# Kernel optimization log

Hardware: AMD Instinct MI355X
Metric: run time of the kernel (lower is better)

Reference implementation:

```python
import jax, jax.numpy as jnp
import numpy as np

N = 1_000_000
G = 32
CLAMP = 1e-4          # sigmoid_clamp
GAMMA = 2.0           # module-level gamma
FOCAL_ALPHA = 0.25    # cfg.MODEL.FCOS.LOSS_ALPHA
FOCAL_GAMMA = 2.0     # cfg.MODEL.FCOS.LOSS_GAMMA


def setup_inputs() -> dict:
    key = jax.random.key(0)
    k1, k2, k3, k4 = jax.random.split(key, 4)
    return {
        "logits_pred": jax.random.normal(k1, (N, 1), dtype=jnp.float32),
        "scores": jax.random.uniform(k2, (N, 1), dtype=jnp.float32),
        "IoUMap": jax.random.uniform(k3, (N, 1), dtype=jnp.float32),
        "is_in_boxes": jax.random.randint(k4, (N, G), 0, 2, dtype=jnp.int32),
        "num_pos_avg": 100,
    }


def reference(logits_pred, scores, IoUMap, is_in_boxes, num_pos_avg):
    f32 = jnp.float32
    mask = is_in_boxes > 0                                  # [N,G] bool
    any_mask = mask.any(axis=0)                             # [G]

    p = jnp.clip(jax.nn.sigmoid(logits_pred), CLAMP, 1.0 - CLAMP)  # box_pred [N,1]
    p0 = p[:, 0]                                            # [N]

    # alignment metrics: single class => scores[:, labels] broadcasts column 0
    am = scores[:, 0][:, None] * mask.astype(f32)           # [N,G]
    iou = jax.lax.stop_gradient(IoUMap)[:, 0][:, None] * mask.astype(f32)

    # per-box confidence = max of alignment metric over in-box locations
    conf = jnp.max(jnp.where(mask, am, -jnp.inf), axis=0)   # [G]
    conf = jnp.where(any_mask, conf, f32(0.0))

    am_safe = jnp.where(mask, am, f32(1.0))                 # avoid pow(0, c) grad issues
    raw = jnp.where(mask, jnp.power(am_safe, conf[None, :]) * iou, f32(0.0))

    # normalize(x) = (x + 1e-4) / (max(x) + 1e-4) over in-box subset
    mx = jnp.max(jnp.where(mask, raw, -jnp.inf), axis=0)    # [G]
    mx = jnp.where(any_mask, mx, f32(1.0))
    pos_w = jnp.where(mask & any_mask[None, :],
                      (raw + CLAMP) / (mx[None, :] + CLAMP), f32(0.0))  # [N,G]

    # negative mask: locations covered by no gt box (single-class case)
    neg_mask = ~mask.any(axis=1)                            # [N]
    neg_loss = jnp.sum(jnp.where(neg_mask,
                                 -jnp.log(1.0 - p0) * jnp.power(p0, FOCAL_GAMMA),
                                 f32(0.0))) * (1.0 - FOCAL_ALPHA)

    wmask = pos_w > 0.0
    wc = jnp.clip(pos_w, CLAMP, 1.0 - CLAMP)                # clamp applied at positive entries
    logp = jnp.log(p0)[:, None]
    log1mp = jnp.log(1.0 - p0)[:, None]
    pos_loss = -jnp.sum(jnp.where(wmask,
                                  logp * jnp.power(wc * (1.0 - p0)[:, None], GAMMA),
                                  f32(0.0))) * FOCAL_ALPHA
    box_neg_loss = -jnp.sum(jnp.where(wmask,
                                      log1mp * jnp.power((1.0 - wc) * p0[:, None], GAMMA),
                                      f32(0.0))) * FOCAL_ALPHA

    denom = jnp.asarray(num_pos_avg, f32)
    return (neg_loss + pos_loss + box_neg_loss) / denom
```

## Files before the change

kernel.cpp:

```cpp
#include <hip/hip_runtime.h>
#include <hip/hip_bf16.h>
#include <stdint.h>


constexpr float kClamp = 1e-4f;
constexpr uint32_t kNegInfKey = 0x007FFFFFu;

__device__ inline uint32_t fkey(float f) {
    uint32_t u = __float_as_uint(f);
    return (u & 0x80000000u) ? ~u : (u | 0x80000000u);
}
__device__ inline float funkey(uint32_t k) {
    uint32_t u = (k & 0x80000000u) ? (k ^ 0x80000000u) : ~k;
    return __uint_as_float(u);
}

__global__ void init_kernel(uint32_t* confbits, uint32_t* mxkeys, float* out) {
    int t = threadIdx.x;
    if (t < 32) { confbits[t] = 0u; mxkeys[t] = kNegInfKey; }
    if (t == 0) out[0] = 0.0f;
}

template <bool WRITE_BITS>
__global__ void pack_conf_kernel(const int4* __restrict__ boxes4,
                                 const float* __restrict__ scores,
                                 uint32_t* __restrict__ bits,
                                 uint32_t* __restrict__ confbits,
                                 long long nchunks) {
    __shared__ uint32_t conf_lds[32];
    int tid = threadIdx.x;
    if (tid < 32) conf_lds[tid] = 0u;
    __syncthreads();
    int g0 = (tid & 7) * 4;
    float r0 = 0.0f, r1 = 0.0f, r2 = 0.0f, r3 = 0.0f;
    long long stride = (long long)gridDim.x * blockDim.x;
    for (long long c = (long long)blockIdx.x * blockDim.x + tid; c < nchunks; c += stride) {
        int4 v = boxes4[c];
        uint32_t nib = (uint32_t)(v.x > 0) | ((uint32_t)(v.y > 0) << 1) |
                       ((uint32_t)(v.z > 0) << 2) | ((uint32_t)(v.w > 0) << 3);
        long long row = c >> 3;
        if (WRITE_BITS) {
            uint32_t r = nib << ((tid & 7) * 4);
            r |= __shfl_xor(r, 1);
            r |= __shfl_xor(r, 2);
            r |= __shfl_xor(r, 4);
            if ((tid & 7) == 0) bits[row] = r;
        }
        float s = scores[row];
        r0 = (nib & 1u) ? fmaxf(r0, s) : r0;
        r1 = (nib & 2u) ? fmaxf(r1, s) : r1;
        r2 = (nib & 4u) ? fmaxf(r2, s) : r2;
        r3 = (nib & 8u) ? fmaxf(r3, s) : r3;
    }
    for (int off = 8; off < 64; off <<= 1) {
        r0 = fmaxf(r0, __shfl_xor(r0, off));
        r1 = fmaxf(r1, __shfl_xor(r1, off));
        r2 = fmaxf(r2, __shfl_xor(r2, off));
        r3 = fmaxf(r3, __shfl_xor(r3, off));
    }
    if ((tid & 63) < 8) {
        atomicMax(&conf_lds[g0 + 0], __float_as_uint(r0));
        atomicMax(&conf_lds[g0 + 1], __float_as_uint(r1));
        atomicMax(&conf_lds[g0 + 2], __float_as_uint(r2));
        atomicMax(&conf_lds[g0 + 3], __float_as_uint(r3));
    }
    __syncthreads();
    if (tid < 32 && conf_lds[tid]) atomicMax(&confbits[tid], conf_lds[tid]);
}

__device__ inline uint32_t row_mask_from_boxes(const int4* __restrict__ boxes4, int row) {
    uint32_t m = 0;
#pragma unroll
    for (int k = 0; k < 8; ++k) {
        int4 v = boxes4[(long long)row * 8 + k];
        uint32_t nib = (uint32_t)(v.x > 0) | ((uint32_t)(v.y > 0) << 1) |
                       ((uint32_t)(v.z > 0) << 2) | ((uint32_t)(v.w > 0) << 3);
        m |= nib << (k * 4);
    }
    return m;
}

template <bool USE_BITS>
__global__ void mx_kernel(const uint32_t* __restrict__ bits,
                          const int4* __restrict__ boxes4,
                          const float* __restrict__ scores,
                          const float* __restrict__ iouMap,
                          const uint32_t* __restrict__ confbits,
                          uint32_t* __restrict__ mxkeys, int n) {
    __shared__ float conf_s[32];
    __shared__ float smax_w[4][32];
    int tid = threadIdx.x;
    if (tid < 32) conf_s[tid] = __uint_as_float(confbits[tid]);
    __syncthreads();
    int chunk = tid & 3;
    float cf[8];
#pragma unroll
    for (int k = 0; k < 8; ++k) cf[k] = conf_s[chunk * 8 + k];
    float lmax[8];
#pragma unroll
    for (int k = 0; k < 8; ++k) lmax[k] = -__builtin_inff();

    int slots = (gridDim.x * blockDim.x) >> 2;
    for (int row = (blockIdx.x * blockDim.x + tid) >> 2; row < n; row += slots) {
        uint32_t m = USE_BITS ? bits[row] : row_mask_from_boxes(boxes4, row);
        uint32_t mc = (m >> (chunk * 8)) & 0xFFu;
        if (!mc) continue;
        float l2s = log2f(scores[row]);
        float l2i = log2f(iouMap[row]);
#pragma unroll
        for (int k = 0; k < 8; ++k) {
            float t0 = cf[k] * l2s;
            t0 = (t0 != t0) ? 0.0f : t0;
            float t = t0 + l2i;
            lmax[k] = (mc & (1u << k)) ? fmaxf(lmax[k], t) : lmax[k];
        }
    }
#pragma unroll
    for (int off = 4; off < 64; off <<= 1) {
#pragma unroll
        for (int k = 0; k < 8; ++k) lmax[k] = fmaxf(lmax[k], __shfl_xor(lmax[k], off));
    }
    int wave = tid >> 6, lane = tid & 63;
    if (lane < 4) {
#pragma unroll
        for (int k = 0; k < 8; ++k) smax_w[wave][lane * 8 + k] = lmax[k];
    }
    __syncthreads();
    if (tid < 32) {
        float v = fmaxf(fmaxf(smax_w[0][tid], smax_w[1][tid]),
                        fmaxf(smax_w[2][tid], smax_w[3][tid]));
        uint32_t k = fkey(v);
        if (k != kNegInfKey) atomicMax(&mxkeys[tid], k);
    }
}

template <bool USE_BITS>
__global__ void loss_kernel(const uint32_t* __restrict__ bits,
                            const int4* __restrict__ boxes4,
                            const float* __restrict__ logits,
                            const float* __restrict__ scores,
                            const float* __restrict__ iouMap,
                            const uint32_t* __restrict__ confbits,
                            const uint32_t* __restrict__ mxkeys,
                            const void* __restrict__ denom_ptr,
                            float* __restrict__ out, int n) {
    __shared__ float conf_s[32];
    __shared__ float invmx[32];
    __shared__ float wsum[4];
    int tid = threadIdx.x;
    if (tid < 32) {
        conf_s[tid] = __uint_as_float(confbits[tid]);
        float mx = exp2f(funkey(mxkeys[tid]));
        invmx[tid] = 1.0f / (mx + kClamp);
    }
    __syncthreads();
    float acc = 0.0f;
    int stride = gridDim.x * blockDim.x;
    for (int row = blockIdx.x * blockDim.x + tid; row < n; row += stride) {
        uint32_t m = USE_BITS ? bits[row] : row_mask_from_boxes(boxes4, row);
        float x = logits[row];
        float p = 1.0f / (1.0f + expf(-x));
        p = fminf(fmaxf(p, kClamp), 1.0f - kClamp);
        if (!m) {
            acc -= logf(1.0f - p) * p * p * 0.75f;
            continue;
        }
        float l2s = log2f(scores[row]);
        float l2i = log2f(iouMap[row]);
        float logp = logf(p);
        float log1mp = logf(1.0f - p);
        float omp = 1.0f - p;
        while (m) {
            int g = __ffs(m) - 1;
            m &= m - 1;
            float t0 = conf_s[g] * l2s;
            t0 = (t0 != t0) ? 0.0f : t0;
            float raw = exp2f(t0 + l2i);
            float wc = (raw + kClamp) * invmx[g];
            wc = fminf(fmaxf(wc, kClamp), 1.0f - kClamp);
            float a1 = wc * omp;
            float a2 = (1.0f - wc) * p;
            acc -= (logp * a1 * a1 + log1mp * a2 * a2) * 0.25f;
        }
    }
    for (int off = 32; off > 0; off >>= 1) acc += __shfl_down(acc, off);
    if ((tid & 63) == 0) wsum[tid >> 6] = acc;
    __syncthreads();
    if (tid == 0) {
        int iv = *(const int*)denom_ptr;
        float fv = *(const float*)denom_ptr;
        float denom = (iv > 0 && iv < (1 << 24)) ? (float)iv : fv;
        float tot = (wsum[0] + wsum[1] + wsum[2] + wsum[3]) / denom;
        atomicAdd(out, tot);
    }
}

extern "C" void kernel_launch(void* const* d_in, const int* in_sizes, int n_in,
                              void* d_out, int out_size, void* d_ws, size_t ws_size,
                              hipStream_t stream) {
    const float* logits = (const float*)d_in[0];
    const float* scores = (const float*)d_in[1];
    const float* iou    = (const float*)d_in[2];
    const int4*  boxes4 = (const int4*)d_in[3];
    const void*  npa    = d_in[4];
    float* out = (float*)d_out;

    int n = in_sizes[0];
    long long gtotal = in_sizes[3];
    long long nchunks = gtotal / 4;

    uint32_t* confbits = (uint32_t*)d_ws;
    uint32_t* mxkeys   = confbits + 32;
    uint32_t* bits     = confbits + 64;
    bool use_bits = ws_size >= (size_t)n * 4 + 256;

    init_kernel<<<1, 64, 0, stream>>>(confbits, mxkeys, out);

    if (use_bits) {
        pack_conf_kernel<true><<<2048, 256, 0, stream>>>(boxes4, scores, bits, confbits, nchunks);
        mx_kernel<true><<<512, 256, 0, stream>>>(bits, nullptr, scores, iou, confbits, mxkeys, n);
        loss_kernel<true><<<1024, 256, 0, stream>>>(bits, nullptr, logits, scores, iou,
                                                    confbits, mxkeys, npa, out, n);
    } else {
        pack_conf_kernel<false><<<2048, 256, 0, stream>>>(boxes4, scores, nullptr, confbits, nchunks);
        mx_kernel<false><<<512, 256, 0, stream>>>(nullptr, boxes4, scores, iou, confbits, mxkeys, n);
        loss_kernel<false><<<1024, 256, 0, stream>>>(nullptr, boxes4, logits, scores, iou,
                                                     confbits, mxkeys, npa, out, n);
    }
}
```

Before: 279.2 us.

## Fuse four launches into one cooperative kernel with grid-wide syncs

Replaces the init, pack/conf, mx and loss kernel chain with a single cooperative kernel that runs the same phases separated by grid.sync. Global atomics are replaced by per-block partial buffers that every block re-reduces after each sync, and the final sum is written deterministically by block 0. The aim is to remove launch gaps and atomic contention. In exchange it adds three grid-wide barriers and redundant partial reductions in every block, and requires all 1024 blocks to be co-resident, falling back to the old path if the cooperative launch fails.

Measured after the change: 771.4 us. 176% more time.

```diff
diff --git a/kernel.cpp b/kernel.cpp
--- a/kernel.cpp
+++ b/kernel.cpp
@@ -1,6 +1,9 @@
 #include <hip/hip_runtime.h>
+#include <hip/hip_cooperative_groups.h>
 #include <hip/hip_bf16.h>
 #include <stdint.h>
+
+namespace cg = cooperative_groups;
 
 
 constexpr float kClamp = 1e-4f;
@@ -13,6 +16,199 @@
 __device__ inline float funkey(uint32_t k) {
     uint32_t u = (k & 0x80000000u) ? (k ^ 0x80000000u) : ~k;
     return __uint_as_float(u);
+}
+
+__global__ __launch_bounds__(256, 4)
+void fused_kernel(const float* __restrict__ logits,
+                  const float* __restrict__ scores,
+                  const float* __restrict__ iouMap,
+                  const int4*  __restrict__ boxes4,
+                  const void*  __restrict__ denom_ptr,
+                  float* __restrict__ out,
+                  float* __restrict__ conf_part,
+                  float* __restrict__ mx_part,
+                  float* __restrict__ lsum,
+                  uint32_t* __restrict__ bits,
+                  int n, long long nchunks) {
+    cg::grid_group grid = cg::this_grid();
+    __shared__ uint32_t conf_u[32];
+    __shared__ float conf_s[32];
+    __shared__ float invmx[32];
+    __shared__ float smax_w[4][32];
+    __shared__ float red[32][33];
+    __shared__ float wsum[4];
+    const int tid = threadIdx.x;
+    const int bid = blockIdx.x;
+    const int nb  = gridDim.x;
+    const long long nthreads = (long long)nb * blockDim.x;
+
+    if (tid < 32) conf_u[tid] = 0u;
+    __syncthreads();
+    {
+        const int g0 = (tid & 7) * 4;
+        float r0 = 0.f, r1 = 0.f, r2 = 0.f, r3 = 0.f;
+        for (long long c = (long long)bid * blockDim.x + tid; c < nchunks; c += nthreads) {
+            int4 v = boxes4[c];
+            uint32_t nib = (uint32_t)(v.x > 0) | ((uint32_t)(v.y > 0) << 1) |
+                           ((uint32_t)(v.z > 0) << 2) | ((uint32_t)(v.w > 0) << 3);
+            long long row = c >> 3;
+            uint32_t r = nib << ((tid & 7) * 4);
+            r |= __shfl_xor(r, 1);
+            r |= __shfl_xor(r, 2);
+            r |= __shfl_xor(r, 4);
+            if ((tid & 7) == 0) bits[row] = r;
+            float s = scores[row];
+            r0 = (nib & 1u) ? fmaxf(r0, s) : r0;
+            r1 = (nib & 2u) ? fmaxf(r1, s) : r1;
+            r2 = (nib & 4u) ? fmaxf(r2, s) : r2;
+            r3 = (nib & 8u) ? fmaxf(r3, s) : r3;
+        }
+        for (int off = 8; off < 64; off <<= 1) {
+            r0 = fmaxf(r0, __shfl_xor(r0, off));
+            r1 = fmaxf(r1, __shfl_xor(r1, off));
+            r2 = fmaxf(r2, __shfl_xor(r2, off));
+            r3 = fmaxf(r3, __shfl_xor(r3, off));
+        }
+        if ((tid & 63) < 8) {
+            atomicMax(&conf_u[g0 + 0], __float_as_uint(r0));
+            atomicMax(&conf_u[g0 + 1], __float_as_uint(r1));
+            atomicMax(&conf_u[g0 + 2], __float_as_uint(r2));
+            atomicMax(&conf_u[g0 + 3], __float_as_uint(r3));
+        }
+        __syncthreads();
+        if (tid < 32) conf_part[bid * 32 + tid] = __uint_as_float(conf_u[tid]);
+    }
+    __threadfence();
+    grid.sync();
+
+    {
+        const float4* cp4 = (const float4*)conf_part;
+        float4 m = make_float4(0.f, 0.f, 0.f, 0.f);
+        const int slot = tid & 7, slice = tid >> 3;
+        for (int b = slice; b < nb; b += 32) {
+            float4 v = cp4[b * 8 + slot];
+            m.x = fmaxf(m.x, v.x); m.y = fmaxf(m.y, v.y);
+            m.z = fmaxf(m.z, v.z); m.w = fmaxf(m.w, v.w);
+        }
+        red[slice][slot * 4 + 0] = m.x; red[slice][slot * 4 + 1] = m.y;
+        red[slice][slot * 4 + 2] = m.z; red[slice][slot * 4 + 3] = m.w;
+        __syncthreads();
+        if (tid < 32) {
+            float v = red[0][tid];
+            for (int s = 1; s < 32; ++s) v = fmaxf(v, red[s][tid]);
+            conf_s[tid] = v;
+        }
+        __syncthreads();
+    }
+
+    {
+        const int chunk = tid & 3;
+        float cf[8], lmax[8];
+#pragma unroll
+        for (int k = 0; k < 8; ++k) { cf[k] = conf_s[chunk * 8 + k]; lmax[k] = -__builtin_inff(); }
+        const int slots = (int)(nthreads >> 2);
+        for (int row = (bid * blockDim.x + tid) >> 2; row < n; row += slots) {
+            uint32_t mc = (bits[row] >> (chunk * 8)) & 0xFFu;
+            if (!mc) continue;
+            float l2s = log2f(scores[row]);
+            float l2i = log2f(iouMap[row]);
+#pragma unroll
+            for (int k = 0; k < 8; ++k) {
+                float t0 = cf[k] * l2s;
+                t0 = (t0 != t0) ? 0.0f : t0;
+                float t = t0 + l2i;
+                lmax[k] = (mc & (1u << k)) ? fmaxf(lmax[k], t) : lmax[k];
+            }
+        }
+#pragma unroll
+        for (int off = 4; off < 64; off <<= 1) {
+#pragma unroll
+            for (int k = 0; k < 8; ++k) lmax[k] = fmaxf(lmax[k], __shfl_xor(lmax[k], off));
+        }
+        const int wave = tid >> 6, lane = tid & 63;
+        if (lane < 4) {
+#pragma unroll
+            for (int k = 0; k < 8; ++k) smax_w[wave][lane * 8 + k] = lmax[k];
+        }
+        __syncthreads();
+        if (tid < 32)
+            mx_part[bid * 32 + tid] = fmaxf(fmaxf(smax_w[0][tid], smax_w[1][tid]),
+                                            fmaxf(smax_w[2][tid], smax_w[3][tid]));
+    }
+    __threadfence();
+    grid.sync();
+
+    {
+        const float4* mp4 = (const float4*)mx_part;
+        const float ninf = -__builtin_inff();
+        float4 m = make_float4(ninf, ninf, ninf, ninf);
+        const int slot = tid & 7, slice = tid >> 3;
+        for (int b = slice; b < nb; b += 32) {
+            float4 v = mp4[b * 8 + slot];
+            m.x = fmaxf(m.x, v.x); m.y = fmaxf(m.y, v.y);
+            m.z = fmaxf(m.z, v.z); m.w = fmaxf(m.w, v.w);
+        }
+        red[slice][slot * 4 + 0] = m.x; red[slice][slot * 4 + 1] = m.y;
+        red[slice][slot * 4 + 2] = m.z; red[slice][slot * 4 + 3] = m.w;
+        __syncthreads();
+        if (tid < 32) {
+            float v = red[0][tid];
+            for (int s = 1; s < 32; ++s) v = fmaxf(v, red[s][tid]);
+            invmx[tid] = 1.0f / (exp2f(v) + kClamp);
+        }
+        __syncthreads();
+    }
+
+    {
+        float acc = 0.0f;
+        for (long long row = (long long)bid * blockDim.x + tid; row < n; row += nthreads) {
+            uint32_t m = bits[row];
+            float x = logits[row];
+            float p = 1.0f / (1.0f + expf(-x));
+            p = fminf(fmaxf(p, kClamp), 1.0f - kClamp);
+            if (!m) {
+                acc -= logf(1.0f - p) * p * p * 0.75f;
+                continue;
+            }
+            float l2s = log2f(scores[row]);
+            float l2i = log2f(iouMap[row]);
+            float logp = logf(p);
+            float log1mp = logf(1.0f - p);
+            float omp = 1.0f - p;
+            while (m) {
+                int g = __ffs(m) - 1;
+                m &= m - 1;
+                float t0 = conf_s[g] * l2s;
+                t0 = (t0 != t0) ? 0.0f : t0;
+                float raw = exp2f(t0 + l2i);
+                float wc = (raw + kClamp) * invmx[g];
+                wc = fminf(fmaxf(wc, kClamp), 1.0f - kClamp);
+                float a1 = wc * omp;
+                float a2 = (1.0f - wc) * p;
+                acc -= (logp * a1 * a1 + log1mp * a2 * a2) * 0.25f;
+            }
+        }
+        for (int off = 32; off > 0; off >>= 1) acc += __shfl_down(acc, off);
+        if ((tid & 63) == 0) wsum[tid >> 6] = acc;
+        __syncthreads();
+        if (tid == 0) lsum[bid] = wsum[0] + wsum[1] + wsum[2] + wsum[3];
+    }
+    __threadfence();
+    grid.sync();
+
+    if (bid == 0) {
+        float a = 0.f;
+        for (int i = tid; i < nb; i += blockDim.x) a += lsum[i];
+        for (int off = 32; off > 0; off >>= 1) a += __shfl_down(a, off);
+        if ((tid & 63) == 0) wsum[tid >> 6] = a;
+        __syncthreads();
+        if (tid == 0) {
+            int iv = *(const int*)denom_ptr;
+            float fv = *(const float*)denom_ptr;
+            float denom = (iv > 0 && iv < (1 << 24)) ? (float)iv : fv;
+            out[0] = (wsum[0] + wsum[1] + wsum[2] + wsum[3]) / denom;
+        }
+    }
 }
 
 __global__ void init_kernel(uint32_t* confbits, uint32_t* mxkeys, float* out) {
@@ -93,13 +289,9 @@
     if (tid < 32) conf_s[tid] = __uint_as_float(confbits[tid]);
     __syncthreads();
     int chunk = tid & 3;
-    float cf[8];
-#pragma unroll
-    for (int k = 0; k < 8; ++k) cf[k] = conf_s[chunk * 8 + k];
-    float lmax[8];
-#pragma unroll
-    for (int k = 0; k < 8; ++k) lmax[k] = -__builtin_inff();
-
+    float cf[8], lmax[8];
+#pragma unroll
+    for (int k = 0; k < 8; ++k) { cf[k] = conf_s[chunk * 8 + k]; lmax[k] = -__builtin_inff(); }
     int slots = (gridDim.x * blockDim.x) >> 2;
     for (int row = (blockIdx.x * blockDim.x + tid) >> 2; row < n; row += slots) {
         uint32_t m = USE_BITS ? bits[row] : row_mask_from_boxes(boxes4, row);
@@ -206,8 +398,24 @@
     float* out = (float*)d_out;
 
     int n = in_sizes[0];
-    long long gtotal = in_sizes[3];
-    long long nchunks = gtotal / 4;
+    long long nchunks = (long long)in_sizes[3] / 4;
+
+    const int nb = 1024, nt = 256;
+    float* conf_part = (float*)d_ws;
+    float* mx_part   = conf_part + nb * 32;
+    float* lsum      = mx_part + nb * 32;
+    uint32_t* bits_f = (uint32_t*)(lsum + nb);
+    size_t need = sizeof(float) * (size_t)(nb * 64 + nb) + sizeof(uint32_t) * (size_t)n;
+
+    if (ws_size >= need) {
+        void* args[] = { (void*)&logits, (void*)&scores, (void*)&iou, (void*)&boxes4,
+                         (void*)&npa, (void*)&out, (void*)&conf_part, (void*)&mx_part,
+                         (void*)&lsum, (void*)&bits_f, (void*)&n, (void*)&nchunks };
+        hipError_t e = hipLaunchCooperativeKernel((const void*)fused_kernel,
+                                                  dim3(nb), dim3(nt), args, 0, stream);
+        if (e == hipSuccess) return;
+        (void)hipGetLastError();
+    }
 
     uint32_t* confbits = (uint32_t*)d_ws;
     uint32_t* mxkeys   = confbits + 32;
@@ -215,7 +423,6 @@
     bool use_bits = ws_size >= (size_t)n * 4 + 256;
 
     init_kernel<<<1, 64, 0, stream>>>(confbits, mxkeys, out);
-
     if (use_bits) {
         pack_conf_kernel<true><<<2048, 256, 0, stream>>>(boxes4, scores, bits, confbits, nchunks);
         mx_kernel<true><<<512, 256, 0, stream>>>(bits, nullptr, scores, iou, confbits, mxkeys, n);
```
